# Optimization experiments

Measured on AMD Instinct MI355X. Metric: run time of the kernel, lower is better.

## Reference

```python
import jax, jax.numpy as jnp
import numpy as np

N_NODES = 100000
N_EDGES = 1600000
HIDDEN = 128
OUT = 64
NUM_LAYERS = 3


def setup_inputs() -> dict:
    key = jax.random.key(0)
    k1, k2, k3 = jax.random.split(key, 3)
    x = jax.random.normal(k1, (N_NODES, HIDDEN), dtype=jnp.float32)
    edge_index = jax.random.randint(k2, (2, N_EDGES), 0, N_NODES, dtype=jnp.int64)
    W = jax.random.normal(k3, (OUT, HIDDEN), dtype=jnp.float32) * (1.0 / np.sqrt(HIDDEN))
    b = jnp.zeros((OUT,), dtype=jnp.float32)
    return {"x": x, "edge_index": edge_index, "W": W, "b": b}


def reference(x, edge_index, W, b):
    n = x.shape[0]
    row, col = edge_index[0], edge_index[1]
    # degree of destination nodes (bincount over row), clamped to >= 1
    deg = jax.ops.segment_sum(jnp.ones_like(row, dtype=x.dtype), row, num_segments=n)
    deg_inv_sqrt = jnp.clip(deg, 1.0, None) ** -0.5
    norm = (deg_inv_sqrt[row] * deg_inv_sqrt[col])[:, None]  # [E, 1]

    def propagate(h):
        # gather -> scale -> scatter-add
        return jax.ops.segment_sum(h[col] * norm, row, num_segments=n)

    embs = [x]
    h = x
    for _ in range(NUM_LAYERS):
        h = propagate(h)
        embs.append(h)
    out = jnp.mean(jnp.stack(embs, axis=0), axis=0)  # [N, HIDDEN]
    return out @ W.T + b
```

## Files before the change

### kernel.cpp

```cpp
#include <hip/hip_runtime.h>

#define N_NODES 100000
#define N_EDGES 1600000
#define HIDDEN  128
#define OUTF    64
#define SLOT    48

__device__ __forceinline__ unsigned short f2bf(float f) {
    unsigned u = __float_as_uint(f);
    u += 0x7fffu + ((u >> 16) & 1u);
    return (unsigned short)(u >> 16);
}
__device__ __forceinline__ float2 bfp2f(unsigned p) {
    return make_float2(__uint_as_float(p << 16), __uint_as_float(p & 0xffff0000u));
}

__global__ void zero_kernel(int4* p, int n4) {
    int i = blockIdx.x * blockDim.x + threadIdx.x;
    if (i < n4) p[i] = make_int4(0, 0, 0, 0);
}

__global__ void zero_dummy_kernel(int4* z0d, int4* z1d, int4* z2d) {
    int t = threadIdx.x;
    if (t < 8)       z0d[t]      = make_int4(0, 0, 0, 0);
    else if (t < 16) z1d[t - 8]  = make_int4(0, 0, 0, 0);
    else if (t < 24) z2d[t - 16] = make_int4(0, 0, 0, 0);
}

__global__ void count_kernel(const int* __restrict__ ei,
                             int* __restrict__ cnt,
                             int* __restrict__ rank) {
    int t  = blockIdx.x * blockDim.x + threadIdx.x;
    int e0 = t * 4;
    if (e0 + 3 < N_EDGES) {
        int4 r4 = *(const int4*)(ei + e0);
        int k0 = atomicAdd(&cnt[r4.x], 1);
        int k1 = atomicAdd(&cnt[r4.y], 1);
        int k2 = atomicAdd(&cnt[r4.z], 1);
        int k3 = atomicAdd(&cnt[r4.w], 1);
        *(int4*)(rank + e0) = make_int4(k0, k1, k2, k3);
    } else {
        for (int e = e0; e < N_EDGES; ++e) rank[e] = atomicAdd(&cnt[ei[e]], 1);
    }
}

__global__ void fill_kernel(const int* __restrict__ ei,
                            const int* __restrict__ rank,
                            int* __restrict__ csr) {
    int t  = blockIdx.x * blockDim.x + threadIdx.x;
    int e0 = t * 4;
    if (e0 + 3 < N_EDGES) {
        int4 r4 = *(const int4*)(ei + e0);
        int4 c4 = *(const int4*)(ei + N_EDGES + e0);
        int4 k4 = *(const int4*)(rank + e0);
        if (k4.x < SLOT) csr[r4.x * SLOT + k4.x] = c4.x;
        if (k4.y < SLOT) csr[r4.y * SLOT + k4.y] = c4.y;
        if (k4.z < SLOT) csr[r4.z * SLOT + k4.z] = c4.z;
        if (k4.w < SLOT) csr[r4.w * SLOT + k4.w] = c4.w;
    } else {
        for (int e = e0; e < N_EDGES; ++e) {
            int k = rank[e];
            if (k < SLOT) csr[ei[e] * SLOT + k] = ei[N_EDGES + e];
        }
    }
}

__global__ void finalize_pad_kernel(const int* __restrict__ cnt,
                                    float* __restrict__ dinv,
                                    float* __restrict__ rdinv,
                                    int* __restrict__ csr) {
    int i = blockIdx.x * blockDim.x + threadIdx.x;
    if (i < N_NODES) {
        int deg  = cnt[i];
        float d  = fmaxf((float)deg, 1.0f);
        dinv[i]  = rsqrtf(d);
        rdinv[i] = sqrtf(d);
        int dc = deg > SLOT ? SLOT : deg;
        int dp = (dc + 7) & ~7;
        #pragma unroll
        for (int j = 0; j < 7; ++j)
            if (dc + j < dp) csr[i * SLOT + dc + j] = N_NODES;
    }
}

__global__ void wtrans_kernel(const float* __restrict__ W, float* __restrict__ Wt) {
    int i = blockIdx.x * blockDim.x + threadIdx.x;
    if (i < HIDDEN * OUTF) {
        int o = i / HIDDEN, k = i % HIDDEN;
        Wt[k * OUTF + o] = W[i];
    }
}

#define GR    64
#define BK    32
#define HSP   36
#define WTP   68
__global__ __launch_bounds__(256) void gemm_kernel(const float* __restrict__ x,
                                                   const float* __restrict__ Wt,
                                                   const float* __restrict__ dinv,
                                                   unsigned short* __restrict__ z0) {
    __shared__ float hs[GR * HSP];
    __shared__ float wt[BK * WTP];
    int tid = threadIdx.x;
    int rowBase = blockIdx.x * GR;

    int o4 = (tid & 15) * 4;
    int rq = (tid >> 4) * 4;
    float4 a0 = {0,0,0,0}, a1 = {0,0,0,0}, a2 = {0,0,0,0}, a3 = {0,0,0,0};

    for (int kt = 0; kt < HIDDEN / BK; ++kt) {
        if (kt) __syncthreads();
        int kbase = kt * BK;
        #pragma unroll
        for (int t = 0; t < 2; ++t) {
            int f = tid + t * 256;
            int r = f >> 3, c4 = (f & 7) * 4;
            int row = rowBase + r;
            float4 v = (row < N_NODES) ? *(const float4*)(x + (size_t)row * HIDDEN + kbase + c4)
                                       : make_float4(0.f, 0.f, 0.f, 0.f);
            *(float4*)&hs[r * HSP + c4] = v;
        }
        #pragma unroll
        for (int t = 0; t < 2; ++t) {
            int f = tid + t * 256;
            int k = f >> 4, c4 = (f & 15) * 4;
            float4 v = *(const float4*)(Wt + (size_t)(kbase + k) * OUTF + c4);
            *(float4*)&wt[k * WTP + c4] = v;
        }
        __syncthreads();
        #pragma unroll 8
        for (int kk = 0; kk < BK; ++kk) {
            float4 wv = *(const float4*)&wt[kk * WTP + o4];
            float h0 = hs[(rq + 0) * HSP + kk];
            float h1 = hs[(rq + 1) * HSP + kk];
            float h2 = hs[(rq + 2) * HSP + kk];
            float h3 = hs[(rq + 3) * HSP + kk];
            a0.x += h0 * wv.x; a0.y += h0 * wv.y; a0.z += h0 * wv.z; a0.w += h0 * wv.w;
            a1.x += h1 * wv.x; a1.y += h1 * wv.y; a1.z += h1 * wv.z; a1.w += h1 * wv.w;
            a2.x += h2 * wv.x; a2.y += h2 * wv.y; a2.z += h2 * wv.z; a2.w += h2 * wv.w;
            a3.x += h3 * wv.x; a3.y += h3 * wv.y; a3.z += h3 * wv.z; a3.w += h3 * wv.w;
        }
    }
    int row = rowBase + rq;
    #pragma unroll
    for (int r = 0; r < 4; ++r) {
        if (row + r < N_NODES) {
            float d = dinv[row + r];
            float4 a = (r == 0) ? a0 : (r == 1) ? a1 : (r == 2) ? a2 : a3;
            ushort4 s = {f2bf(a.x * d), f2bf(a.y * d), f2bf(a.z * d), f2bf(a.w * d)};
            *(ushort4*)&z0[(size_t)(row + r) * OUTF + o4] = s;
        }
    }
}

__global__ __launch_bounds__(256) void pull_kernel(const int* __restrict__ cnt,
                                                   const int* __restrict__ csr,
                                                   const float* __restrict__ dinv,
                                                   const unsigned short* __restrict__ zsrc,
                                                   unsigned short* __restrict__ zdst) {
    int node = blockIdx.x * 4 + (threadIdx.x >> 6);
    int lane = threadIdx.x & 63;
    if (node >= N_NODES) return;
    int half = lane >> 5;
    int fp   = (lane & 31) * 2;
    int deg  = cnt[node];
    if (deg > SLOT) deg = SLOT;
    int degp = (deg + 7) & ~7;
    int s = node * SLOT;
    int e = s + degp;
    float2 acc = make_float2(0.f, 0.f);
    int i = s;
    for (; i + 15 < e; i += 16) {
        int c0 = csr[i      + half];
        int c1 = csr[i +  2 + half];
        int c2 = csr[i +  4 + half];
        int c3 = csr[i +  6 + half];
        int c4 = csr[i +  8 + half];
        int c5 = csr[i + 10 + half];
        int c6 = csr[i + 12 + half];
        int c7 = csr[i + 14 + half];
        unsigned p0 = *(const unsigned*)(zsrc + (size_t)c0 * OUTF + fp);
        unsigned p1 = *(const unsigned*)(zsrc + (size_t)c1 * OUTF + fp);
        unsigned p2 = *(const unsigned*)(zsrc + (size_t)c2 * OUTF + fp);
        unsigned p3 = *(const unsigned*)(zsrc + (size_t)c3 * OUTF + fp);
        unsigned p4 = *(const unsigned*)(zsrc + (size_t)c4 * OUTF + fp);
        unsigned p5 = *(const unsigned*)(zsrc + (size_t)c5 * OUTF + fp);
        unsigned p6 = *(const unsigned*)(zsrc + (size_t)c6 * OUTF + fp);
        unsigned p7 = *(const unsigned*)(zsrc + (size_t)c7 * OUTF + fp);
        float2 v0 = bfp2f(p0), v1 = bfp2f(p1), v2 = bfp2f(p2), v3 = bfp2f(p3);
        float2 v4 = bfp2f(p4), v5 = bfp2f(p5), v6 = bfp2f(p6), v7 = bfp2f(p7);
        acc.x += (v0.x + v1.x) + (v2.x + v3.x) + (v4.x + v5.x) + (v6.x + v7.x);
        acc.y += (v0.y + v1.y) + (v2.y + v3.y) + (v4.y + v5.y) + (v6.y + v7.y);
    }
    if (i < e) {
        int c0 = csr[i     + half];
        int c1 = csr[i + 2 + half];
        int c2 = csr[i + 4 + half];
        int c3 = csr[i + 6 + half];
        unsigned p0 = *(const unsigned*)(zsrc + (size_t)c0 * OUTF + fp);
        unsigned p1 = *(const unsigned*)(zsrc + (size_t)c1 * OUTF + fp);
        unsigned p2 = *(const unsigned*)(zsrc + (size_t)c2 * OUTF + fp);
        unsigned p3 = *(const unsigned*)(zsrc + (size_t)c3 * OUTF + fp);
        float2 v0 = bfp2f(p0), v1 = bfp2f(p1), v2 = bfp2f(p2), v3 = bfp2f(p3);
        acc.x += (v0.x + v1.x) + (v2.x + v3.x);
        acc.y += (v0.y + v1.y) + (v2.y + v3.y);
    }
    acc.x += __shfl_xor(acc.x, 32);
    acc.y += __shfl_xor(acc.y, 32);
    if (lane < 32) {
        float dn = dinv[node];
        float zs = dn * dn;
        ushort2 o = {f2bf(acc.x * zs), f2bf(acc.y * zs)};
        *(ushort2*)(zdst + (size_t)node * OUTF + fp) = o;
    }
}

__global__ __launch_bounds__(256) void pull_merge_kernel(const int* __restrict__ cnt,
                                                         const int* __restrict__ csr,
                                                         const float* __restrict__ dinv,
                                                         const float* __restrict__ rdinv,
                                                         const unsigned short* __restrict__ z0,
                                                         const unsigned short* __restrict__ z1,
                                                         const unsigned short* __restrict__ z2,
                                                         const float* __restrict__ b,
                                                         float* __restrict__ out) {
    int node = blockIdx.x * 4 + (threadIdx.x >> 6);
    int lane = threadIdx.x & 63;
    if (node >= N_NODES) return;
    int half = lane >> 5;
    int fp   = (lane & 31) * 2;
    int deg  = cnt[node];
    if (deg > SLOT) deg = SLOT;
    int degp = (deg + 7) & ~7;
    int s = node * SLOT;
    int e = s + degp;
    float2 acc = make_float2(0.f, 0.f);
    int i = s;
    for (; i + 15 < e; i += 16) {
        int c0 = csr[i      + half];
        int c1 = csr[i +  2 + half];
        int c2 = csr[i +  4 + half];
        int c3 = csr[i +  6 + half];
        int c4 = csr[i +  8 + half];
        int c5 = csr[i + 10 + half];
        int c6 = csr[i + 12 + half];
        int c7 = csr[i + 14 + half];
        unsigned p0 = *(const unsigned*)(z2 + (size_t)c0 * OUTF + fp);
        unsigned p1 = *(const unsigned*)(z2 + (size_t)c1 * OUTF + fp);
        unsigned p2 = *(const unsigned*)(z2 + (size_t)c2 * OUTF + fp);
        unsigned p3 = *(const unsigned*)(z2 + (size_t)c3 * OUTF + fp);
        unsigned p4 = *(const unsigned*)(z2 + (size_t)c4 * OUTF + fp);
        unsigned p5 = *(const unsigned*)(z2 + (size_t)c5 * OUTF + fp);
        unsigned p6 = *(const unsigned*)(z2 + (size_t)c6 * OUTF + fp);
        unsigned p7 = *(const unsigned*)(z2 + (size_t)c7 * OUTF + fp);
        float2 v0 = bfp2f(p0), v1 = bfp2f(p1), v2 = bfp2f(p2), v3 = bfp2f(p3);
        float2 v4 = bfp2f(p4), v5 = bfp2f(p5), v6 = bfp2f(p6), v7 = bfp2f(p7);
        acc.x += (v0.x + v1.x) + (v2.x + v3.x) + (v4.x + v5.x) + (v6.x + v7.x);
        acc.y += (v0.y + v1.y) + (v2.y + v3.y) + (v4.y + v5.y) + (v6.y + v7.y);
    }
    if (i < e) {
        int c0 = csr[i     + half];
        int c1 = csr[i + 2 + half];
        int c2 = csr[i + 4 + half];
        int c3 = csr[i + 6 + half];
        unsigned p0 = *(const unsigned*)(z2 + (size_t)c0 * OUTF + fp);
        unsigned p1 = *(const unsigned*)(z2 + (size_t)c1 * OUTF + fp);
        unsigned p2 = *(const unsigned*)(z2 + (size_t)c2 * OUTF + fp);
        unsigned p3 = *(const unsigned*)(z2 + (size_t)c3 * OUTF + fp);
        float2 v0 = bfp2f(p0), v1 = bfp2f(p1), v2 = bfp2f(p2), v3 = bfp2f(p3);
        acc.x += (v0.x + v1.x) + (v2.x + v3.x);
        acc.y += (v0.y + v1.y) + (v2.y + v3.y);
    }
    acc.x += __shfl_xor(acc.x, 32);
    acc.y += __shfl_xor(acc.y, 32);
    if (lane < 32) {
        size_t idx = (size_t)node * OUTF + fp;
        float rd = rdinv[node];
        float dn = dinv[node];
        float2 s0 = bfp2f(*(const unsigned*)(z0 + idx));
        float2 s1 = bfp2f(*(const unsigned*)(z1 + idx));
        float2 s2 = bfp2f(*(const unsigned*)(z2 + idx));
        float2 bv = *(const float2*)(b + fp);
        float2 r;
        r.x = 0.25f * ((s0.x + s1.x + s2.x) * rd + dn * acc.x) + bv.x;
        r.y = 0.25f * ((s0.y + s1.y + s2.y) * rd + dn * acc.y) + bv.y;
        *(float2*)(out + idx) = r;
    }
}

extern "C" void kernel_launch(void* const* d_in, const int* in_sizes, int n_in,
                              void* d_out, int out_size, void* d_ws, size_t ws_size,
                              hipStream_t stream) {
    const float* x  = (const float*)d_in[0];
    const int*   ei = (const int*)d_in[1];
    const float* W  = (const float*)d_in[2];
    const float* b  = (const float*)d_in[3];
    float*       out = (float*)d_out;

    const size_t ZROWS = (size_t)N_NODES + 1;
    unsigned short* z0 = (unsigned short*)d_ws;
    unsigned short* z1 = z0 + ZROWS * OUTF;
    unsigned short* z2 = z1 + ZROWS * OUTF;
    float* Wt      = (float*)(z2 + ZROWS * OUTF);
    int*   csr     = (int*)(Wt + HIDDEN * OUTF);
    int*   cnt     = csr + (size_t)N_NODES * SLOT;
    float* dinv    = (float*)(cnt + N_NODES);
    float* rdinv   = dinv + N_NODES;

    int* rank = (int*)z2;

    const int BLK = 256;
    const int edge4Blocks = (N_EDGES / 4 + BLK - 1) / BLK;
    const int nodeBlocks  = (N_NODES + BLK - 1) / BLK;
    const int cntZero4    = (N_NODES / 4 + BLK - 1) / BLK;
    const int pullBlocks  = (N_NODES + 3) / 4;
    const int gemmBlocks  = (N_NODES + GR - 1) / GR;

    zero_kernel<<<cntZero4, BLK, 0, stream>>>((int4*)cnt, N_NODES / 4);
    count_kernel<<<edge4Blocks, BLK, 0, stream>>>(ei, cnt, rank);
    fill_kernel<<<edge4Blocks, BLK, 0, stream>>>(ei, rank, csr);
    finalize_pad_kernel<<<nodeBlocks, BLK, 0, stream>>>(cnt, dinv, rdinv, csr);
    zero_dummy_kernel<<<1, 32, 0, stream>>>((int4*)(z0 + (size_t)N_NODES * OUTF),
                                            (int4*)(z1 + (size_t)N_NODES * OUTF),
                                            (int4*)(z2 + (size_t)N_NODES * OUTF));

    wtrans_kernel<<<(HIDDEN * OUTF + BLK - 1) / BLK, BLK, 0, stream>>>(W, Wt);
    gemm_kernel<<<gemmBlocks, BLK, 0, stream>>>(x, Wt, dinv, z0);
    pull_kernel<<<pullBlocks, BLK, 0, stream>>>(cnt, csr, dinv, z0, z1);
    pull_kernel<<<pullBlocks, BLK, 0, stream>>>(cnt, csr, dinv, z1, z2);
    pull_merge_kernel<<<pullBlocks, BLK, 0, stream>>>(cnt, csr, dinv, rdinv,
                                                      z0, z1, z2, b, out);
}
```

Baseline: 331.7 us.

## Fuse graph-build kernels and overlap edge counting with the GEMM

Replaces the nine-launch pipeline with six launches. The zeroing, W transpose and dummy-row clearing become one prep kernel. The degree count now runs in the odd blocks of the GEMM launch, and the CSR fill shares a launch with degree finalize and padding. This works because the GEMM no longer applies the dinv scaling. Instead the first pull layer multiplies each gathered neighbour by its dinv, which adds a per-edge dinv gather, and the merge kernel rescales the y0 self term. The goal is fewer launches and overlap of atomic-bound counting with compute-bound GEMM work, at the cost of extra dinv gathers in layer 1.

```diff
diff --git a/kernel.cpp b/kernel.cpp
--- a/kernel.cpp
+++ b/kernel.cpp
@@ -6,6 +6,9 @@
 #define OUTF    64
 #define SLOT    48
 
+#define EDGE4BLKS ((N_EDGES / 4 + 255) / 256)
+#define NODEBLKS  ((N_NODES + 255) / 256)
+
 __device__ __forceinline__ unsigned short f2bf(float f) {
     unsigned u = __float_as_uint(f);
     u += 0x7fffu + ((u >> 16) & 1u);
@@ -15,79 +18,24 @@
     return make_float2(__uint_as_float(p << 16), __uint_as_float(p & 0xffff0000u));
 }
 
-__global__ void zero_kernel(int4* p, int n4) {
-    int i = blockIdx.x * blockDim.x + threadIdx.x;
-    if (i < n4) p[i] = make_int4(0, 0, 0, 0);
-}
-
-__global__ void zero_dummy_kernel(int4* z0d, int4* z1d, int4* z2d) {
-    int t = threadIdx.x;
-    if (t < 8)       z0d[t]      = make_int4(0, 0, 0, 0);
-    else if (t < 16) z1d[t - 8]  = make_int4(0, 0, 0, 0);
-    else if (t < 24) z2d[t - 16] = make_int4(0, 0, 0, 0);
-}
-
-__global__ void count_kernel(const int* __restrict__ ei,
-                             int* __restrict__ cnt,
-                             int* __restrict__ rank) {
-    int t  = blockIdx.x * blockDim.x + threadIdx.x;
-    int e0 = t * 4;
-    if (e0 + 3 < N_EDGES) {
-        int4 r4 = *(const int4*)(ei + e0);
-        int k0 = atomicAdd(&cnt[r4.x], 1);
-        int k1 = atomicAdd(&cnt[r4.y], 1);
-        int k2 = atomicAdd(&cnt[r4.z], 1);
-        int k3 = atomicAdd(&cnt[r4.w], 1);
-        *(int4*)(rank + e0) = make_int4(k0, k1, k2, k3);
+__global__ void prep_kernel(const float* __restrict__ W, float* __restrict__ Wt,
+                            int4* __restrict__ cnt4,
+                            int4* __restrict__ z0d, int4* __restrict__ z1d,
+                            int4* __restrict__ z2d) {
+    int bid = blockIdx.x, tid = threadIdx.x;
+    if (bid < 98) {
+        int i = bid * 256 + tid;
+        if (i < N_NODES / 4) cnt4[i] = make_int4(0, 0, 0, 0);
+    } else if (bid < 130) {
+        int i = (bid - 98) * 256 + tid;
+        if (i < HIDDEN * OUTF) {
+            int o = i / HIDDEN, k = i % HIDDEN;
+            Wt[k * OUTF + o] = W[i];
+        }
     } else {
-        for (int e = e0; e < N_EDGES; ++e) rank[e] = atomicAdd(&cnt[ei[e]], 1);
-    }
-}
-
-__global__ void fill_kernel(const int* __restrict__ ei,
-                            const int* __restrict__ rank,
-                            int* __restrict__ csr) {
-    int t  = blockIdx.x * blockDim.x + threadIdx.x;
-    int e0 = t * 4;
-    if (e0 + 3 < N_EDGES) {
-        int4 r4 = *(const int4*)(ei + e0);
-        int4 c4 = *(const int4*)(ei + N_EDGES + e0);
-        int4 k4 = *(const int4*)(rank + e0);
-        if (k4.x < SLOT) csr[r4.x * SLOT + k4.x] = c4.x;
-        if (k4.y < SLOT) csr[r4.y * SLOT + k4.y] = c4.y;
-        if (k4.z < SLOT) csr[r4.z * SLOT + k4.z] = c4.z;
-        if (k4.w < SLOT) csr[r4.w * SLOT + k4.w] = c4.w;
-    } else {
-        for (int e = e0; e < N_EDGES; ++e) {
-            int k = rank[e];
-            if (k < SLOT) csr[ei[e] * SLOT + k] = ei[N_EDGES + e];
-        }
-    }
-}
-
-__global__ void finalize_pad_kernel(const int* __restrict__ cnt,
-                                    float* __restrict__ dinv,
-                                    float* __restrict__ rdinv,
-                                    int* __restrict__ csr) {
-    int i = blockIdx.x * blockDim.x + threadIdx.x;
-    if (i < N_NODES) {
-        int deg  = cnt[i];
-        float d  = fmaxf((float)deg, 1.0f);
-        dinv[i]  = rsqrtf(d);
-        rdinv[i] = sqrtf(d);
-        int dc = deg > SLOT ? SLOT : deg;
-        int dp = (dc + 7) & ~7;
-        #pragma unroll
-        for (int j = 0; j < 7; ++j)
-            if (dc + j < dp) csr[i * SLOT + dc + j] = N_NODES;
-    }
-}
-
-__global__ void wtrans_kernel(const float* __restrict__ W, float* __restrict__ Wt) {
-    int i = blockIdx.x * blockDim.x + threadIdx.x;
-    if (i < HIDDEN * OUTF) {
-        int o = i / HIDDEN, k = i % HIDDEN;
-        Wt[k * OUTF + o] = W[i];
+        if (tid < 8)       z0d[tid]      = make_int4(0, 0, 0, 0);
+        else if (tid < 16) z1d[tid - 8]  = make_int4(0, 0, 0, 0);
+        else if (tid < 24) z2d[tid - 16] = make_int4(0, 0, 0, 0);
     }
 }
 
@@ -95,15 +43,34 @@
 #define BK    32
 #define HSP   36
 #define WTP   68
-__global__ __launch_bounds__(256) void gemm_kernel(const float* __restrict__ x,
-                                                   const float* __restrict__ Wt,
-                                                   const float* __restrict__ dinv,
-                                                   unsigned short* __restrict__ z0) {
+__global__ __launch_bounds__(256) void mega_a_kernel(const float* __restrict__ x,
+                                                     const float* __restrict__ Wt,
+                                                     unsigned short* __restrict__ y0,
+                                                     const int* __restrict__ ei,
+                                                     int* __restrict__ cnt,
+                                                     int* __restrict__ rank) {
     __shared__ float hs[GR * HSP];
     __shared__ float wt[BK * WTP];
     int tid = threadIdx.x;
-    int rowBase = blockIdx.x * GR;
-
+
+    if (blockIdx.x & 1) {
+        int cb = blockIdx.x >> 1;
+        int t  = cb * 256 + tid;
+        int e0 = t * 4;
+        if (e0 + 3 < N_EDGES) {
+            int4 r4 = *(const int4*)(ei + e0);
+            int k0 = atomicAdd(&cnt[r4.x], 1);
+            int k1 = atomicAdd(&cnt[r4.y], 1);
+            int k2 = atomicAdd(&cnt[r4.z], 1);
+            int k3 = atomicAdd(&cnt[r4.w], 1);
+            *(int4*)(rank + e0) = make_int4(k0, k1, k2, k3);
+        } else {
+            for (int e = e0; e < N_EDGES; ++e) rank[e] = atomicAdd(&cnt[ei[e]], 1);
+        }
+        return;
+    }
+
+    int rowBase = (blockIdx.x >> 1) * GR;
     int o4 = (tid & 15) * 4;
     int rq = (tid >> 4) * 4;
     float4 a0 = {0,0,0,0}, a1 = {0,0,0,0}, a2 = {0,0,0,0}, a3 = {0,0,0,0};
@@ -145,11 +112,116 @@
     #pragma unroll
     for (int r = 0; r < 4; ++r) {
         if (row + r < N_NODES) {
-            float d = dinv[row + r];
             float4 a = (r == 0) ? a0 : (r == 1) ? a1 : (r == 2) ? a2 : a3;
-            ushort4 s = {f2bf(a.x * d), f2bf(a.y * d), f2bf(a.z * d), f2bf(a.w * d)};
-            *(ushort4*)&z0[(size_t)(row + r) * OUTF + o4] = s;
-        }
+            ushort4 s = {f2bf(a.x), f2bf(a.y), f2bf(a.z), f2bf(a.w)};
+            *(ushort4*)&y0[(size_t)(row + r) * OUTF + o4] = s;
+        }
+    }
+}
+
+__global__ void mega_b_kernel(const int* __restrict__ ei,
+                              const int* __restrict__ rank,
+                              int* __restrict__ csr,
+                              const int* __restrict__ cnt,
+                              float* __restrict__ dinv,
+                              float* __restrict__ rdinv) {
+    int bid = blockIdx.x, tid = threadIdx.x;
+    if (bid < EDGE4BLKS) {
+        int t  = bid * 256 + tid;
+        int e0 = t * 4;
+        if (e0 + 3 < N_EDGES) {
+            int4 r4 = *(const int4*)(ei + e0);
+            int4 c4 = *(const int4*)(ei + N_EDGES + e0);
+            int4 k4 = *(const int4*)(rank + e0);
+            if (k4.x < SLOT) csr[r4.x * SLOT + k4.x] = c4.x;
+            if (k4.y < SLOT) csr[r4.y * SLOT + k4.y] = c4.y;
+            if (k4.z < SLOT) csr[r4.z * SLOT + k4.z] = c4.z;
+            if (k4.w < SLOT) csr[r4.w * SLOT + k4.w] = c4.w;
+        } else {
+            for (int e = e0; e < N_EDGES; ++e) {
+                int k = rank[e];
+                if (k < SLOT) csr[ei[e] * SLOT + k] = ei[N_EDGES + e];
+            }
+        }
+    } else {
+        int i = (bid - EDGE4BLKS) * 256 + tid;
+        if (i < N_NODES) {
+            int deg  = cnt[i];
+            float d  = fmaxf((float)deg, 1.0f);
+            dinv[i]  = rsqrtf(d);
+            rdinv[i] = sqrtf(d);
+            if (i == 0) dinv[N_NODES] = 0.0f;
+            int dc = deg > SLOT ? SLOT : deg;
+            int dp = (dc + 7) & ~7;
+            #pragma unroll
+            for (int j = 0; j < 7; ++j)
+                if (dc + j < dp) csr[i * SLOT + dc + j] = N_NODES;
+        }
+    }
+}
+
+__global__ __launch_bounds__(256) void pull1_kernel(const int* __restrict__ cnt,
+                                                    const int* __restrict__ csr,
+                                                    const float* __restrict__ dinv,
+                                                    const unsigned short* __restrict__ y0,
+                                                    unsigned short* __restrict__ z1) {
+    int node = blockIdx.x * 4 + (threadIdx.x >> 6);
+    int lane = threadIdx.x & 63;
+    if (node >= N_NODES) return;
+    int half = lane >> 5;
+    int fp   = (lane & 31) * 2;
+    int deg  = cnt[node];
+    if (deg > SLOT) deg = SLOT;
+    int degp = (deg + 7) & ~7;
+    int s = node * SLOT;
+    int e = s + degp;
+    float2 acc = make_float2(0.f, 0.f);
+    int i = s;
+    for (; i + 15 < e; i += 16) {
+        int c0 = csr[i      + half];
+        int c1 = csr[i +  2 + half];
+        int c2 = csr[i +  4 + half];
+        int c3 = csr[i +  6 + half];
+        int c4 = csr[i +  8 + half];
+        int c5 = csr[i + 10 + half];
+        int c6 = csr[i + 12 + half];
+        int c7 = csr[i + 14 + half];
+        float d0 = dinv[c0], d1 = dinv[c1], d2 = dinv[c2], d3 = dinv[c3];
+        float d4 = dinv[c4], d5 = dinv[c5], d6 = dinv[c6], d7 = dinv[c7];
+        unsigned p0 = *(const unsigned*)(y0 + (size_t)c0 * OUTF + fp);
+        unsigned p1 = *(const unsigned*)(y0 + (size_t)c1 * OUTF + fp);
+        unsigned p2 = *(const unsigned*)(y0 + (size_t)c2 * OUTF + fp);
+        unsigned p3 = *(const unsigned*)(y0 + (size_t)c3 * OUTF + fp);
+        unsigned p4 = *(const unsigned*)(y0 + (size_t)c4 * OUTF + fp);
+        unsigned p5 = *(const unsigned*)(y0 + (size_t)c5 * OUTF + fp);
+        unsigned p6 = *(const unsigned*)(y0 + (size_t)c6 * OUTF + fp);
+        unsigned p7 = *(const unsigned*)(y0 + (size_t)c7 * OUTF + fp);
+        float2 v0 = bfp2f(p0), v1 = bfp2f(p1), v2 = bfp2f(p2), v3 = bfp2f(p3);
+        float2 v4 = bfp2f(p4), v5 = bfp2f(p5), v6 = bfp2f(p6), v7 = bfp2f(p7);
+        acc.x += d0*v0.x + d1*v1.x + d2*v2.x + d3*v3.x + d4*v4.x + d5*v5.x + d6*v6.x + d7*v7.x;
+        acc.y += d0*v0.y + d1*v1.y + d2*v2.y + d3*v3.y + d4*v4.y + d5*v5.y + d6*v6.y + d7*v7.y;
+    }
+    if (i < e) {
+        int c0 = csr[i     + half];
+        int c1 = csr[i + 2 + half];
+        int c2 = csr[i + 4 + half];
+        int c3 = csr[i + 6 + half];
+        float d0 = dinv[c0], d1 = dinv[c1], d2 = dinv[c2], d3 = dinv[c3];
+        unsigned p0 = *(const unsigned*)(y0 + (size_t)c0 * OUTF + fp);
+        unsigned p1 = *(const unsigned*)(y0 + (size_t)c1 * OUTF + fp);
+        unsigned p2 = *(const unsigned*)(y0 + (size_t)c2 * OUTF + fp);
+        unsigned p3 = *(const unsigned*)(y0 + (size_t)c3 * OUTF + fp);
+        float2 v0 = bfp2f(p0), v1 = bfp2f(p1), v2 = bfp2f(p2), v3 = bfp2f(p3);
+        acc.x += d0*v0.x + d1*v1.x + d2*v2.x + d3*v3.x;
+        acc.y += d0*v0.y + d1*v1.y + d2*v2.y + d3*v3.y;
+    }
+    acc.x += __shfl_xor(acc.x, 32);
+    acc.y += __shfl_xor(acc.y, 32);
+    if (lane < 32) {
+        float dn = dinv[node];
+        float zs = dn * dn;
+        ushort2 o = {f2bf(acc.x * zs), f2bf(acc.y * zs)};
+        *(ushort2*)(z1 + (size_t)node * OUTF + fp) = o;
     }
 }
 
@@ -219,7 +291,7 @@
                                                          const int* __restrict__ csr,
                                                          const float* __restrict__ dinv,
                                                          const float* __restrict__ rdinv,
-                                                         const unsigned short* __restrict__ z0,
+                                                         const unsigned short* __restrict__ y0,
                                                          const unsigned short* __restrict__ z1,
                                                          const unsigned short* __restrict__ z2,
                                                          const float* __restrict__ b,
@@ -277,13 +349,13 @@
         size_t idx = (size_t)node * OUTF + fp;
         float rd = rdinv[node];
         float dn = dinv[node];
-        float2 s0 = bfp2f(*(const unsigned*)(z0 + idx));
+        float2 s0 = bfp2f(*(const unsigned*)(y0 + idx));
         float2 s1 = bfp2f(*(const unsigned*)(z1 + idx));
         float2 s2 = bfp2f(*(const unsigned*)(z2 + idx));
         float2 bv = *(const float2*)(b + fp);
         float2 r;
-        r.x = 0.25f * ((s0.x + s1.x + s2.x) * rd + dn * acc.x) + bv.x;
-        r.y = 0.25f * ((s0.y + s1.y + s2.y) * rd + dn * acc.y) + bv.y;
+        r.x = 0.25f * ((dn * s0.x + s1.x + s2.x) * rd + dn * acc.x) + bv.x;
+        r.y = 0.25f * ((dn * s0.y + s1.y + s2.y) * rd + dn * acc.y) + bv.y;
         *(float2*)(out + idx) = r;
     }
 }
@@ -298,36 +370,28 @@
     float*       out = (float*)d_out;
 
     const size_t ZROWS = (size_t)N_NODES + 1;
-    unsigned short* z0 = (unsigned short*)d_ws;
-    unsigned short* z1 = z0 + ZROWS * OUTF;
+    unsigned short* y0 = (unsigned short*)d_ws;
+    unsigned short* z1 = y0 + ZROWS * OUTF;
     unsigned short* z2 = z1 + ZROWS * OUTF;
     float* Wt      = (float*)(z2 + ZROWS * OUTF);
     int*   csr     = (int*)(Wt + HIDDEN * OUTF);
     int*   cnt     = csr + (size_t)N_NODES * SLOT;
     float* dinv    = (float*)(cnt + N_NODES);
-    float* rdinv   = dinv + N_NODES;
+    float* rdinv   = dinv + (N_NODES + 1);
 
     int* rank = (int*)z2;
 
     const int BLK = 256;
-    const int edge4Blocks = (N_EDGES / 4 + BLK - 1) / BLK;
-    const int nodeBlocks  = (N_NODES + BLK - 1) / BLK;
-    const int cntZero4    = (N_NODES / 4 + BLK - 1) / BLK;
-    const int pullBlocks  = (N_NODES + 3) / 4;
-    const int gemmBlocks  = (N_NODES + GR - 1) / GR;
-
-    zero_kernel<<<cntZero4, BLK, 0, stream>>>((int4*)cnt, N_NODES / 4);
-    count_kernel<<<edge4Blocks, BLK, 0, stream>>>(ei, cnt, rank);
-    fill_kernel<<<edge4Blocks, BLK, 0, stream>>>(ei, rank, csr);
-    finalize_pad_kernel<<<nodeBlocks, BLK, 0, stream>>>(cnt, dinv, rdinv, csr);
-    zero_dummy_kernel<<<1, 32, 0, stream>>>((int4*)(z0 + (size_t)N_NODES * OUTF),
-                                            (int4*)(z1 + (size_t)N_NODES * OUTF),
-                                            (int4*)(z2 + (size_t)N_NODES * OUTF));
-
-    wtrans_kernel<<<(HIDDEN * OUTF + BLK - 1) / BLK, BLK, 0, stream>>>(W, Wt);
-    gemm_kernel<<<gemmBlocks, BLK, 0, stream>>>(x, Wt, dinv, z0);
-    pull_kernel<<<pullBlocks, BLK, 0, stream>>>(cnt, csr, dinv, z0, z1);
+    const int pullBlocks = (N_NODES + 3) / 4;
+
+    prep_kernel<<<131, BLK, 0, stream>>>(W, Wt, (int4*)cnt,
+                                         (int4*)(y0 + (size_t)N_NODES * OUTF),
+                                         (int4*)(z1 + (size_t)N_NODES * OUTF),
+                                         (int4*)(z2 + (size_t)N_NODES * OUTF));
+    mega_a_kernel<<<2 * EDGE4BLKS, BLK, 0, stream>>>(x, Wt, y0, ei, cnt, rank);
+    mega_b_kernel<<<EDGE4BLKS + NODEBLKS, BLK, 0, stream>>>(ei, rank, csr, cnt, dinv, rdinv);
+    pull1_kernel<<<pullBlocks, BLK, 0, stream>>>(cnt, csr, dinv, y0, z1);
     pull_kernel<<<pullBlocks, BLK, 0, stream>>>(cnt, csr, dinv, z1, z2);
     pull_merge_kernel<<<pullBlocks, BLK, 0, stream>>>(cnt, csr, dinv, rdinv,
-                                                      z0, z1, z2, b, out);
-}
+                                                      y0, z1, z2, b, out);
+}
```

Result: faster. 297.1 us (-10.4%).
